# Performance work log

Hardware: AMD Instinct MI355X
Metric: run time of the kernel (lower is better)

Reference implementation:

```python
import jax, jax.numpy as jnp
import numpy as np

B = 128        # graph pairs per batch
NPG = 512      # nodes per graph (equal-size graphs -> dense batch is a reshape)
D = 64         # input feature dim
DEG = 16       # avg degree
FILTERS = [64, 32, 16]
RDIM = 10      # resize_dim
CCH = 8        # conv channels per similarity image
MLP = [32, 16, 8, 4, 1]


def _make_edges(rng, n_graphs, npg, deg):
    E = n_graphs * npg * deg
    off = np.repeat(np.arange(n_graphs, dtype=np.int64) * npg, npg * deg)
    src = rng.integers(0, npg, E) + off
    dst = rng.integers(0, npg, E) + off
    return jnp.asarray(np.stack([src, dst]), dtype=jnp.int32)


def setup_inputs() -> dict:
    key = jax.random.key(0)
    ks = jax.random.split(key, 40)
    rng = np.random.default_rng(0)
    N = B * NPG
    inp = {}
    inp['x_i'] = jax.random.normal(ks[0], (N, D), jnp.float32)
    inp['x_j'] = jax.random.normal(ks[1], (N, D), jnp.float32)
    # GCN weights
    dims = [D] + FILTERS
    k = 2
    for li in range(3):
        fi, fo = dims[li], dims[li + 1]
        inp[f'gcn_w{li}'] = jax.random.normal(ks[k], (fi, fo), jnp.float32) / np.sqrt(fi); k += 1
        inp[f'gcn_b{li}'] = jnp.zeros((fo,), jnp.float32)
    # Conv filters: one Conv2d(1->CCH, 3x3, SAME) per GNN layer, OIHW kernels
    for li in range(3):
        inp[f'conv_w{li}'] = jax.random.normal(ks[k], (CCH, 1, 3, 3), jnp.float32) / 3.0; k += 1
        inp[f'conv_b{li}'] = jnp.zeros((CCH,), jnp.float32)
    # MLP (Linear-ReLU stack) + scoring layer
    mdims = [3 * CCH * RDIM * RDIM] + MLP
    for li in range(len(MLP)):
        fi, fo = mdims[li], mdims[li + 1]
        inp[f'mlp_w{li}'] = jax.random.normal(ks[k], (fi, fo), jnp.float32) / np.sqrt(fi); k += 1
        inp[f'mlp_b{li}'] = jnp.zeros((fo,), jnp.float32)
    inp['score_w'] = jax.random.normal(ks[k], (1, 1), jnp.float32); k += 1
    inp['score_b'] = jnp.zeros((1,), jnp.float32)
    # Graph structure (int constants)
    inp['edge_index_i'] = _make_edges(rng, B, NPG, DEG)
    inp['edge_index_j'] = _make_edges(rng, B, NPG, DEG)
    batch = jnp.asarray(np.repeat(np.arange(B, dtype=np.int64), NPG), dtype=jnp.int32)
    inp['batch_i'] = batch
    inp['batch_j'] = batch
    return inp


def _gcn(x, ei, w, b):
    # PyG GCNConv: A_hat = D^-1/2 (A + I) D^-1/2 ; out = A_hat (x W) + b
    src, dst = ei[0], ei[1]
    n = x.shape[0]
    xw = x @ w
    deg = jax.ops.segment_sum(jnp.ones(ei.shape[1], xw.dtype), dst, num_segments=n) + 1.0
    inv = jax.lax.rsqrt(deg)
    msg = xw[src] * (inv[src] * inv[dst])[:, None]
    agg = jax.ops.segment_sum(msg, dst, num_segments=n)
    return agg + xw * (inv * inv)[:, None] + b


def _forward(x_i, x_j, gcn_w0, gcn_b0, gcn_w1, gcn_b1, gcn_w2, gcn_b2,
             conv_w0, conv_b0, conv_w1, conv_b1, conv_w2, conv_b2,
             mlp_w0, mlp_b0, mlp_w1, mlp_b1, mlp_w2, mlp_b2, mlp_w3, mlp_b3, mlp_w4, mlp_b4,
             score_w, score_b, edge_index_i, edge_index_j):
    gws = [(gcn_w0, gcn_b0), (gcn_w1, gcn_b1), (gcn_w2, gcn_b2)]
    cvs = [(conv_w0, conv_b0), (conv_w1, conv_b1), (conv_w2, conv_b2)]
    embs = []
    for li, (w, b) in enumerate(gws):
        x_i = _gcn(x_i, edge_index_i, w, b)
        x_j = _gcn(x_j, edge_index_j, w, b)
        if li != len(gws) - 1:  # activation + dropout (eval mode -> identity)
            x_i = jax.nn.relu(x_i)
            x_j = jax.nn.relu(x_j)
        h_i = x_i.reshape(B, NPG, -1)  # to_dense_batch (equal-size graphs)
        h_j = x_j.reshape(B, NPG, -1)
        sim = jnp.einsum('bnd,bmd->bnm', h_i, h_j)  # [B, NPG, NPG]
        simr = jax.image.resize(sim, (B, RDIM, RDIM), method='bilinear', antialias=False)
        cw, cb = cvs[li]
        y = jax.lax.conv_general_dilated(simr[:, None], cw, (1, 1), 'SAME')
        y = jax.nn.relu(y + cb[None, :, None, None])  # [B, CCH, RDIM, RDIM]
        embs.append(y.reshape(B, -1))
    feat = jnp.concatenate(embs, axis=1)  # [B, 3*CCH*RDIM*RDIM]
    for w, b in [(mlp_w0, mlp_b0), (mlp_w1, mlp_b1), (mlp_w2, mlp_b2), (mlp_w3, mlp_b3), (mlp_w4, mlp_b4)]:
        feat = jax.nn.relu(feat @ w + b)
    score = jax.nn.sigmoid(feat @ score_w + score_b)
    return score.reshape(-1)


def reference(x_i, x_j, gcn_w0, gcn_b0, gcn_w1, gcn_b1, gcn_w2, gcn_b2,
              conv_w0, conv_b0, conv_w1, conv_b1, conv_w2, conv_b2,
              mlp_w0, mlp_b0, mlp_w1, mlp_b1, mlp_w2, mlp_b2, mlp_w3, mlp_b3, mlp_w4, mlp_b4,
              score_w, score_b, edge_index_i, edge_index_j, batch_i, batch_j):
    # batch_i/batch_j are implicit in the block layout (equal-size graphs)
    return _forward(x_i, x_j, gcn_w0, gcn_b0, gcn_w1, gcn_b1, gcn_w2, gcn_b2,
                    conv_w0, conv_b0, conv_w1, conv_b1, conv_w2, conv_b2,
                    mlp_w0, mlp_b0, mlp_w1, mlp_b1, mlp_w2, mlp_b2, mlp_w3, mlp_b3, mlp_w4, mlp_b4,
                    score_w, score_b, edge_index_i, edge_index_j)
```

## Files before the change

kernel.cpp:

```cpp
#include <hip/hip_runtime.h>

typedef float fvec4 __attribute__((ext_vector_type(4)));

#define NN 65536
#define EE 1048576
#define BB 128
#define NPG 512
#define EPG 8192

template <int NQ, int FOUT, int COFF, bool RELU, bool LAST>
__device__ __forceinline__ void pass32(const fvec4* acc, fvec4* o,
                                       const float* __restrict__ bias,
                                       int node, int start, int count, float inv_v, int slot,
                                       fvec4* __restrict__ msgQ, const int* __restrict__ sids,
                                       float* __restrict__ hs, int hb) {
  {
    const int rb = node << 3;
    const int m = node & 7;
#pragma unroll
    for (int q = 0; q < NQ; ++q) msgQ[rb | ((q + m) & 7)] = acc[q] * inv_v;
  }
  __syncthreads();
  if (!LAST || slot >= 0) {
    fvec4 s[NQ];
#pragma unroll
    for (int q = 0; q < NQ; ++q) s[q] = fvec4{0.f, 0.f, 0.f, 0.f};
    int e = start;
    const int end = start + count;
    for (; e + 2 <= end; e += 2) {
      const int k0 = sids[e], k1 = sids[e + 1];
      const int b0 = k0 & ~7, b1 = k1 & ~7;
#pragma unroll
      for (int q = 0; q < NQ; ++q) s[q] += msgQ[b0 | ((q + k0) & 7)];
#pragma unroll
      for (int q = 0; q < NQ; ++q) s[q] += msgQ[b1 | ((q + k1) & 7)];
    }
    if (e < end) {
      const int k0 = sids[e];
      const int b0 = k0 & ~7;
#pragma unroll
      for (int q = 0; q < NQ; ++q) s[q] += msgQ[b0 | ((q + k0) & 7)];
    }
    const float i2 = inv_v * inv_v;
#pragma unroll
    for (int q = 0; q < NQ; ++q) {
#pragma unroll
      for (int j = 0; j < 4; ++j) {
        float ov = s[q][j] * inv_v + acc[q][j] * i2 + bias[COFF + q * 4 + j];
        if (RELU) ov = fmaxf(ov, 0.f);
        o[q][j] = ov;
      }
    }
    if (slot >= 0) {
      fvec4* hp = reinterpret_cast<fvec4*>(hs + ((size_t)hb + slot) * FOUT + COFF);
#pragma unroll
      for (int q = 0; q < NQ; ++q) hp[q] = o[q];
    }
  }
  __syncthreads();
}

__global__ __launch_bounds__(512)
void k_all(const float* __restrict__ x_i, const float* __restrict__ x_j,
           const float* __restrict__ gw0, const float* __restrict__ gb0,
           const float* __restrict__ gw1, const float* __restrict__ gb1,
           const float* __restrict__ gw2, const float* __restrict__ gb2,
           const int* __restrict__ ei, const int* __restrict__ ej,
           float* __restrict__ hs0, float* __restrict__ hs1, float* __restrict__ hs2) {
  __shared__ int sids[EPG];
  __shared__ fvec4 msgQ[NPG * 8];
  __shared__ int cnt[NPG];
  __shared__ int posb[NPG];
  __shared__ int nodeOf[NPG];
  __shared__ int bins[64];
  __shared__ int binpos[64];
  __shared__ int wsum[8];
  int* const dsts = reinterpret_cast<int*>(msgQ);

  const int side = blockIdx.x >> 7;
  const int g = blockIdx.x & 127;
  const float* __restrict__ x = side ? x_j : x_i;
  const int* __restrict__ eidx = side ? ej : ei;
  const int v = threadIdx.x;
  const int base = g * NPG;
  const int ebase = g * EPG;

  cnt[v] = 0;
  if (v < 64) bins[v] = 0;
  __syncthreads();
  for (int k = v; k < EPG; k += 512) {
    int d = eidx[EE + ebase + k] - base;
    dsts[k] = d;
    atomicAdd(&cnt[d], 1);
  }
  __syncthreads();

  const int count = cnt[v];
  const int deg = count > 63 ? 63 : count;
  atomicAdd(&bins[deg], 1);
  int xa = count;
  const int lane = v & 63;
#pragma unroll
  for (int d = 1; d < 64; d <<= 1) {
    int y = __shfl_up(xa, d, 64);
    if (lane >= d) xa += y;
  }
  const int wid = v >> 6;
  if (lane == 63) wsum[wid] = xa;
  __syncthreads();
  if (v < 64) {
    if (v == 0) {
      int a = 0;
#pragma unroll
      for (int i = 0; i < 8; ++i) { int tv = wsum[i]; wsum[i] = a; a += tv; }
    }
    int c = bins[v];
    int xb = c;
#pragma unroll
    for (int d = 1; d < 64; d <<= 1) {
      int y = __shfl_up(xb, d, 64);
      if (v >= d) xb += y;
    }
    binpos[v] = xb - c;
  }
  __syncthreads();
  const int start_v = xa - count + wsum[wid];
  posb[v] = start_v;
  {
    int rank = atomicAdd(&binpos[deg], 1);
    nodeOf[rank] = v;
  }
  __syncthreads();

  for (int k = v; k < EPG; k += 512) {
    int lv = eidx[ebase + k] - base;
    int p = atomicAdd(&posb[dsts[k]], 1);
    sids[p] = (lv << 3) | (lv & 7);
  }
  __syncthreads();

  const int node = nodeOf[v];
  const int ncount = cnt[node];
  const int nstart = posb[node] - ncount;
  const float inv_v = rsqrtf((float)ncount + 1.0f);

  constexpr int srows[20] = {25, 26, 76, 77, 127, 128, 178, 179, 229, 230,
                             281, 282, 332, 333, 383, 384, 434, 435, 485, 486};
  int slot = -1;
#pragma unroll
  for (int i = 0; i < 20; ++i)
    if (node == srows[i]) slot = i;
  const int hb = (side * BB + g) * 20;

  fvec4 a0[16];
#pragma unroll
  for (int q = 0; q < 16; ++q) a0[q] = fvec4{0.f, 0.f, 0.f, 0.f};
  {
    const fvec4* xv = reinterpret_cast<const fvec4*>(x + (size_t)(base + node) * 64);
#pragma unroll 1
    for (int k16 = 0; k16 < 4; ++k16) {
      fvec4 xq[4];
#pragma unroll
      for (int u = 0; u < 4; ++u) xq[u] = xv[4 * k16 + u];
#pragma unroll
      for (int u = 0; u < 4; ++u) {
#pragma unroll
        for (int j = 0; j < 4; ++j) {
          const float xk = xq[u][j];
          const fvec4* wr = reinterpret_cast<const fvec4*>(gw0 + (size_t)(16 * k16 + 4 * u + j) * 64);
#pragma unroll
          for (int q = 0; q < 16; ++q) a0[q] += xk * wr[q];
        }
      }
    }
  }

  fvec4 y1[8];
  {
    fvec4 o[8];
    pass32<8, 64, 0, true, false>(&a0[0], o, gb0, node, nstart, ncount, inv_v, slot, msgQ, sids, hs0, hb);
#pragma unroll
    for (int q = 0; q < 8; ++q) y1[q] = fvec4{0.f, 0.f, 0.f, 0.f};
#pragma unroll
    for (int f = 0; f < 32; ++f) {
      const float hf = o[f >> 2][f & 3];
      const fvec4* wr = reinterpret_cast<const fvec4*>(gw1 + (size_t)f * 32);
#pragma unroll
      for (int q = 0; q < 8; ++q) y1[q] += hf * wr[q];
    }
  }
  {
    fvec4 o[8];
    pass32<8, 64, 32, true, false>(&a0[8], o, gb0, node, nstart, ncount, inv_v, slot, msgQ, sids, hs0, hb);
#pragma unroll
    for (int f = 0; f < 32; ++f) {
      const float hf = o[f >> 2][f & 3];
      const fvec4* wr = reinterpret_cast<const fvec4*>(gw1 + (size_t)(32 + f) * 32);
#pragma unroll
      for (int q = 0; q < 8; ++q) y1[q] += hf * wr[q];
    }
  }

  fvec4 y2[4];
  {
    fvec4 o[8];
    pass32<8, 32, 0, true, false>(y1, o, gb1, node, nstart, ncount, inv_v, slot, msgQ, sids, hs1, hb);
#pragma unroll
    for (int q = 0; q < 4; ++q) y2[q] = fvec4{0.f, 0.f, 0.f, 0.f};
#pragma unroll
    for (int f = 0; f < 32; ++f) {
      const float hf = o[f >> 2][f & 3];
      const fvec4* wr = reinterpret_cast<const fvec4*>(gw2 + (size_t)f * 16);
#pragma unroll
      for (int q = 0; q < 4; ++q) y2[q] += hf * wr[q];
    }
  }

  {
    fvec4 o[4];
    pass32<4, 16, 0, false, true>(y2, o, gb2, node, nstart, ncount, inv_v, slot, msgQ, sids, hs2, hb);
  }
}

__global__ __launch_bounds__(256) void k_head(const float* __restrict__ hs0, const float* __restrict__ hs1,
                                              const float* __restrict__ hs2,
                                              const float* __restrict__ cw0, const float* __restrict__ cb0,
                                              const float* __restrict__ cw1, const float* __restrict__ cb1,
                                              const float* __restrict__ cw2, const float* __restrict__ cb2,
                                              const float* __restrict__ mw0, const float* __restrict__ mb0,
                                              const float* __restrict__ mw1, const float* __restrict__ mb1,
                                              const float* __restrict__ mw2, const float* __restrict__ mb2,
                                              const float* __restrict__ mw3, const float* __restrict__ mb3,
                                              const float* __restrict__ mw4, const float* __restrict__ mb4,
                                              const float* __restrict__ sw, const float* __restrict__ sb,
                                              float* __restrict__ out) {
  __shared__ float hi[2240];
  __shared__ float hj[2240];
  __shared__ float sim[400];
  __shared__ float simr[100];
  __shared__ float feat[2400];
  __shared__ float red[256];
  __shared__ float mbuf[60];
  const int b = blockIdx.x, t = threadIdx.x;

  for (int k = t; k < 1280; k += 256) {
    hi[k] = hs0[(size_t)(0 * BB + b) * 1280 + k];
    hj[k] = hs0[(size_t)(1 * BB + b) * 1280 + k];
  }
  for (int k = t; k < 640; k += 256) {
    hi[1280 + k] = hs1[(size_t)(0 * BB + b) * 640 + k];
    hj[1280 + k] = hs1[(size_t)(1 * BB + b) * 640 + k];
  }
  for (int k = t; k < 320; k += 256) {
    hi[1920 + k] = hs2[(size_t)(0 * BB + b) * 320 + k];
    hj[1920 + k] = hs2[(size_t)(1 * BB + b) * 320 + k];
  }
  __syncthreads();

  const int Fs[3] = {64, 32, 16};
  const int HOFF[3] = {0, 1280, 1920};
  const float* CW[3] = {cw0, cw1, cw2};
  const float* CB[3] = {cb0, cb1, cb2};

  for (int li = 0; li < 3; ++li) {
    const int F = Fs[li];
    const float* Hi = hi + HOFF[li];
    const float* Hj = hj + HOFF[li];
    for (int p = t; p < 400; p += 256) {
      int r = p / 20, cq = p % 20;
      float a = 0.0f;
      for (int d = 0; d < F; ++d) a += Hi[r * F + d] * Hj[cq * F + d];
      sim[p] = a;
    }
    __syncthreads();
    if (t < 100) {
      int oy = t / 10, ox = t % 10;
      float cy = (oy + 0.5f) * (512.0f / 10.0f) - 0.5f;
      float cx = (ox + 0.5f) * (512.0f / 10.0f) - 0.5f;
      float fy = cy - floorf(cy);
      float fx = cx - floorf(cx);
      int r0 = 2 * oy, c0 = 2 * ox;
      float s00 = sim[r0 * 20 + c0], s01 = sim[r0 * 20 + c0 + 1];
      float s10 = sim[(r0 + 1) * 20 + c0], s11 = sim[(r0 + 1) * 20 + c0 + 1];
      simr[t] = (1.0f - fy) * ((1.0f - fx) * s00 + fx * s01) + fy * ((1.0f - fx) * s10 + fx * s11);
    }
    __syncthreads();
    const float* cw = CW[li];
    const float* cb = CB[li];
    for (int idx = t; idx < 800; idx += 256) {
      int cch = idx / 100, rem = idx % 100, y = rem / 10, x = rem % 10;
      float a = cb[cch];
#pragma unroll
      for (int ky = 0; ky < 3; ++ky) {
#pragma unroll
        for (int kx = 0; kx < 3; ++kx) {
          int iy = y + ky - 1, ix = x + kx - 1;
          if (iy >= 0 && iy < 10 && ix >= 0 && ix < 10)
            a += cw[cch * 9 + ky * 3 + kx] * simr[iy * 10 + ix];
        }
      }
      feat[li * 800 + idx] = fmaxf(a, 0.0f);
    }
    __syncthreads();
  }

  {
    int f = t & 31, part = t >> 5;
    float a = 0.0f;
    int k0 = part * 300;
    for (int k = k0; k < k0 + 300; ++k) a += feat[k] * mw0[k * 32 + f];
    red[t] = a;
    __syncthreads();
    if (t < 32) {
      float s = mb0[t];
#pragma unroll
      for (int p = 0; p < 8; ++p) s += red[p * 32 + t];
      mbuf[t] = fmaxf(s, 0.0f);
    }
    __syncthreads();
  }
  if (t < 16) {
    float s = mb1[t];
    for (int k = 0; k < 32; ++k) s += mbuf[k] * mw1[k * 16 + t];
    mbuf[32 + t] = fmaxf(s, 0.0f);
  }
  __syncthreads();
  if (t < 8) {
    float s = mb2[t];
    for (int k = 0; k < 16; ++k) s += mbuf[32 + k] * mw2[k * 8 + t];
    mbuf[48 + t] = fmaxf(s, 0.0f);
  }
  __syncthreads();
  if (t < 4) {
    float s = mb3[t];
    for (int k = 0; k < 8; ++k) s += mbuf[48 + k] * mw3[k * 4 + t];
    mbuf[56 + t] = fmaxf(s, 0.0f);
  }
  __syncthreads();
  if (t == 0) {
    float s = mb4[0];
    for (int k = 0; k < 4; ++k) s += mbuf[56 + k] * mw4[k];
    s = fmaxf(s, 0.0f);
    float z = s * sw[0] + sb[0];
    out[b] = 1.0f / (1.0f + expf(-z));
  }
}

extern "C" void kernel_launch(void* const* d_in, const int* in_sizes, int n_in,
                              void* d_out, int out_size, void* d_ws, size_t ws_size,
                              hipStream_t stream) {
  (void)in_sizes; (void)n_in; (void)out_size; (void)ws_size;
  const float* x_i = (const float*)d_in[0];
  const float* x_j = (const float*)d_in[1];
  const float* gw0 = (const float*)d_in[2];
  const float* gb0 = (const float*)d_in[3];
  const float* gw1 = (const float*)d_in[4];
  const float* gb1 = (const float*)d_in[5];
  const float* gw2 = (const float*)d_in[6];
  const float* gb2 = (const float*)d_in[7];
  const float* cw0 = (const float*)d_in[8];
  const float* cb0 = (const float*)d_in[9];
  const float* cw1 = (const float*)d_in[10];
  const float* cb1 = (const float*)d_in[11];
  const float* cw2 = (const float*)d_in[12];
  const float* cb2 = (const float*)d_in[13];
  const float* mw0 = (const float*)d_in[14];
  const float* mb0 = (const float*)d_in[15];
  const float* mw1 = (const float*)d_in[16];
  const float* mb1 = (const float*)d_in[17];
  const float* mw2 = (const float*)d_in[18];
  const float* mb2 = (const float*)d_in[19];
  const float* mw3 = (const float*)d_in[20];
  const float* mb3 = (const float*)d_in[21];
  const float* mw4 = (const float*)d_in[22];
  const float* mb4 = (const float*)d_in[23];
  const float* scw = (const float*)d_in[24];
  const float* scb = (const float*)d_in[25];
  const int* ei = (const int*)d_in[26];
  const int* ej = (const int*)d_in[27];
  float* out = (float*)d_out;

  char* p = (char*)d_ws;
  auto take = [&](size_t bytes) {
    char* r = p;
    p += (bytes + 255) & ~(size_t)255;
    return r;
  };
  float* hs0 = (float*)take((size_t)2 * BB * 20 * 64 * 4);
  float* hs1 = (float*)take((size_t)2 * BB * 20 * 32 * 4);
  float* hs2 = (float*)take((size_t)2 * BB * 20 * 16 * 4);

  k_all<<<2 * BB, 512, 0, stream>>>(x_i, x_j, gw0, gb0, gw1, gb1, gw2, gb2,
                                    ei, ej, hs0, hs1, hs2);
  k_head<<<BB, 256, 0, stream>>>(hs0, hs1, hs2, cw0, cb0, cw1, cb1, cw2, cb2,
                                 mw0, mb0, mw1, mb1, mw2, mb2, mw3, mb3, mw4, mb4,
                                 scw, scb, out);
}
```

Baseline: 130.5 us.

## Store GCN neighbor messages in fp16 and merge layer-0 aggregation passes

Neighbor messages in shared memory are now packed as half2 instead of fp32, which halves LDS traffic per gather and lets both 32-feature halves of layer 0 be aggregated in one pass over the edge list using two buffers. The self-loop term is folded into the accumulator initialisation, and the sids encoding is changed to address the packed layout. This removes one edge traversal and a pair of barriers. The cost is fp16 rounding of the messages, which may affect accuracy.

Result: no change. 132.4 us (+1.5%).

```diff
diff --git a/kernel.cpp b/kernel.cpp
--- a/kernel.cpp
+++ b/kernel.cpp
@@ -1,6 +1,8 @@
 #include <hip/hip_runtime.h>
+#include <hip/hip_fp16.h>
 
 typedef float fvec4 __attribute__((ext_vector_type(4)));
+typedef int ivec4 __attribute__((ext_vector_type(4)));
 
 #define NN 65536
 #define EE 1048576
@@ -8,56 +10,32 @@
 #define NPG 512
 #define EPG 8192
 
-template <int NQ, int FOUT, int COFF, bool RELU, bool LAST>
-__device__ __forceinline__ void pass32(const fvec4* acc, fvec4* o,
-                                       const float* __restrict__ bias,
-                                       int node, int start, int count, float inv_v, int slot,
-                                       fvec4* __restrict__ msgQ, const int* __restrict__ sids,
-                                       float* __restrict__ hs, int hb) {
-  {
-    const int rb = node << 3;
-    const int m = node & 7;
-#pragma unroll
-    for (int q = 0; q < NQ; ++q) msgQ[rb | ((q + m) & 7)] = acc[q] * inv_v;
-  }
-  __syncthreads();
-  if (!LAST || slot >= 0) {
-    fvec4 s[NQ];
-#pragma unroll
-    for (int q = 0; q < NQ; ++q) s[q] = fvec4{0.f, 0.f, 0.f, 0.f};
-    int e = start;
-    const int end = start + count;
-    for (; e + 2 <= end; e += 2) {
-      const int k0 = sids[e], k1 = sids[e + 1];
-      const int b0 = k0 & ~7, b1 = k1 & ~7;
-#pragma unroll
-      for (int q = 0; q < NQ; ++q) s[q] += msgQ[b0 | ((q + k0) & 7)];
-#pragma unroll
-      for (int q = 0; q < NQ; ++q) s[q] += msgQ[b1 | ((q + k1) & 7)];
-    }
-    if (e < end) {
-      const int k0 = sids[e];
-      const int b0 = k0 & ~7;
-#pragma unroll
-      for (int q = 0; q < NQ; ++q) s[q] += msgQ[b0 | ((q + k0) & 7)];
-    }
-    const float i2 = inv_v * inv_v;
-#pragma unroll
-    for (int q = 0; q < NQ; ++q) {
-#pragma unroll
-      for (int j = 0; j < 4; ++j) {
-        float ov = s[q][j] * inv_v + acc[q][j] * i2 + bias[COFF + q * 4 + j];
-        if (RELU) ov = fmaxf(ov, 0.f);
-        o[q][j] = ov;
-      }
-    }
-    if (slot >= 0) {
-      fvec4* hp = reinterpret_cast<fvec4*>(hs + ((size_t)hb + slot) * FOUT + COFF);
-#pragma unroll
-      for (int q = 0; q < NQ; ++q) hp[q] = o[q];
-    }
-  }
-  __syncthreads();
+__device__ __forceinline__ int pk2(float a, float b) {
+  union { __half2 h; int i; } u; u.h = __floats2half2_rn(a, b); return u.i;
+}
+__device__ __forceinline__ float2 up2(int v) {
+  union { int i; __half2 h; } u; u.i = v; return __half22float2(u.h);
+}
+
+#define ACCQ(S, w) { float2 f_; \
+  f_ = up2((w)[0]); (S)[0][0] += f_.x; (S)[0][1] += f_.y; \
+  f_ = up2((w)[1]); (S)[0][2] += f_.x; (S)[0][3] += f_.y; \
+  f_ = up2((w)[2]); (S)[1][0] += f_.x; (S)[1][1] += f_.y; \
+  f_ = up2((w)[3]); (S)[1][2] += f_.x; (S)[1][3] += f_.y; }
+
+__device__ __forceinline__ void pub32(const fvec4* acc, float inv_v, int node, ivec4* buf) {
+  const int line = node >> 1;
+  const int m = ((node & 1) << 2) + (line & 7);
+  const int b = line << 3;
+#pragma unroll
+  for (int q = 0; q < 4; ++q) {
+    fvec4 a0 = acc[2 * q] * inv_v;
+    fvec4 a1 = acc[2 * q + 1] * inv_v;
+    ivec4 w;
+    w[0] = pk2(a0[0], a0[1]); w[1] = pk2(a0[2], a0[3]);
+    w[2] = pk2(a1[0], a1[1]); w[3] = pk2(a1[2], a1[3]);
+    buf[b | ((q + m) & 7)] = w;
+  }
 }
 
 __global__ __launch_bounds__(512)
@@ -68,14 +46,15 @@
            const int* __restrict__ ei, const int* __restrict__ ej,
            float* __restrict__ hs0, float* __restrict__ hs1, float* __restrict__ hs2) {
   __shared__ int sids[EPG];
-  __shared__ fvec4 msgQ[NPG * 8];
+  __shared__ ivec4 bufA[(NPG / 2) * 8];
+  __shared__ ivec4 bufB[(NPG / 2) * 8];
   __shared__ int cnt[NPG];
   __shared__ int posb[NPG];
   __shared__ int nodeOf[NPG];
   __shared__ int bins[64];
   __shared__ int binpos[64];
   __shared__ int wsum[8];
-  int* const dsts = reinterpret_cast<int*>(msgQ);
+  int* const dsts = reinterpret_cast<int*>(bufA);
 
   const int side = blockIdx.x >> 7;
   const int g = blockIdx.x & 127;
@@ -135,7 +114,9 @@
   for (int k = v; k < EPG; k += 512) {
     int lv = eidx[ebase + k] - base;
     int p = atomicAdd(&posb[dsts[k]], 1);
-    sids[p] = (lv << 3) | (lv & 7);
+    int line = lv >> 1;
+    int m = ((lv & 1) << 2) + (line & 7);
+    sids[p] = (line << 4) | m;
   }
   __syncthreads();
 
@@ -175,50 +156,123 @@
     }
   }
 
+  pub32(&a0[0], inv_v, node, bufA);
+  pub32(&a0[8], inv_v, node, bufB);
+  fvec4 sA[8], sB[8];
+#pragma unroll
+  for (int q = 0; q < 8; ++q) { sA[q] = a0[q] * inv_v; sB[q] = a0[8 + q] * inv_v; }
+  __syncthreads();
+
+  {
+    const int end = nstart + ncount;
+    for (int e = nstart; e < end; ++e) {
+      const int key = sids[e];
+      const int b = (key >> 1) & ~7;
+#pragma unroll
+      for (int q = 0; q < 4; ++q) {
+        const int idx = b | ((q + key) & 7);
+        const ivec4 wa = bufA[idx];
+        const ivec4 wb = bufB[idx];
+        ACCQ((&sA[2 * q]), wa)
+        ACCQ((&sB[2 * q]), wb)
+      }
+    }
+  }
+
   fvec4 y1[8];
-  {
-    fvec4 o[8];
-    pass32<8, 64, 0, true, false>(&a0[0], o, gb0, node, nstart, ncount, inv_v, slot, msgQ, sids, hs0, hb);
-#pragma unroll
-    for (int q = 0; q < 8; ++q) y1[q] = fvec4{0.f, 0.f, 0.f, 0.f};
-#pragma unroll
-    for (int f = 0; f < 32; ++f) {
-      const float hf = o[f >> 2][f & 3];
-      const fvec4* wr = reinterpret_cast<const fvec4*>(gw1 + (size_t)f * 32);
-#pragma unroll
-      for (int q = 0; q < 8; ++q) y1[q] += hf * wr[q];
-    }
-  }
-  {
-    fvec4 o[8];
-    pass32<8, 64, 32, true, false>(&a0[8], o, gb0, node, nstart, ncount, inv_v, slot, msgQ, sids, hs0, hb);
-#pragma unroll
-    for (int f = 0; f < 32; ++f) {
-      const float hf = o[f >> 2][f & 3];
-      const fvec4* wr = reinterpret_cast<const fvec4*>(gw1 + (size_t)(32 + f) * 32);
-#pragma unroll
-      for (int q = 0; q < 8; ++q) y1[q] += hf * wr[q];
-    }
-  }
-
+#pragma unroll
+  for (int p = 0; p < 8; ++p) y1[p] = fvec4{0.f, 0.f, 0.f, 0.f};
+  {
+    const fvec4* gb0v = reinterpret_cast<const fvec4*>(gb0);
+    fvec4* hp = reinterpret_cast<fvec4*>(hs0 + ((size_t)hb + slot) * 64);
+#pragma unroll
+    for (int q = 0; q < 16; ++q) {
+      fvec4 s = (q < 8) ? sA[q] : sB[q - 8];
+      fvec4 o = s * inv_v + gb0v[q];
+#pragma unroll
+      for (int j = 0; j < 4; ++j) o[j] = fmaxf(o[j], 0.f);
+      if (slot >= 0) hp[q] = o;
+#pragma unroll
+      for (int j = 0; j < 4; ++j) {
+        const float hf = o[j];
+        const fvec4* wr = reinterpret_cast<const fvec4*>(gw1 + (size_t)(q * 4 + j) * 32);
+#pragma unroll
+        for (int p = 0; p < 8; ++p) y1[p] += hf * wr[p];
+      }
+    }
+  }
+  __syncthreads();
+
+  pub32(y1, inv_v, node, bufA);
+  fvec4 s1[8];
+#pragma unroll
+  for (int q = 0; q < 8; ++q) s1[q] = y1[q] * inv_v;
+  __syncthreads();
+  {
+    const int end = nstart + ncount;
+    for (int e = nstart; e < end; ++e) {
+      const int key = sids[e];
+      const int b = (key >> 1) & ~7;
+#pragma unroll
+      for (int q = 0; q < 4; ++q) {
+        const ivec4 w = bufA[b | ((q + key) & 7)];
+        ACCQ((&s1[2 * q]), w)
+      }
+    }
+  }
   fvec4 y2[4];
-  {
-    fvec4 o[8];
-    pass32<8, 32, 0, true, false>(y1, o, gb1, node, nstart, ncount, inv_v, slot, msgQ, sids, hs1, hb);
-#pragma unroll
-    for (int q = 0; q < 4; ++q) y2[q] = fvec4{0.f, 0.f, 0.f, 0.f};
-#pragma unroll
-    for (int f = 0; f < 32; ++f) {
-      const float hf = o[f >> 2][f & 3];
-      const fvec4* wr = reinterpret_cast<const fvec4*>(gw2 + (size_t)f * 16);
-#pragma unroll
-      for (int q = 0; q < 4; ++q) y2[q] += hf * wr[q];
-    }
-  }
-
-  {
-    fvec4 o[4];
-    pass32<4, 16, 0, false, true>(y2, o, gb2, node, nstart, ncount, inv_v, slot, msgQ, sids, hs2, hb);
+#pragma unroll
+  for (int p = 0; p < 4; ++p) y2[p] = fvec4{0.f, 0.f, 0.f, 0.f};
+  {
+    const fvec4* gb1v = reinterpret_cast<const fvec4*>(gb1);
+    fvec4* hp = reinterpret_cast<fvec4*>(hs1 + ((size_t)hb + slot) * 32);
+#pragma unroll
+    for (int q = 0; q < 8; ++q) {
+      fvec4 o = s1[q] * inv_v + gb1v[q];
+#pragma unroll
+      for (int j = 0; j < 4; ++j) o[j] = fmaxf(o[j], 0.f);
+      if (slot >= 0) hp[q] = o;
+#pragma unroll
+      for (int j = 0; j < 4; ++j) {
+        const float hf = o[j];
+        const fvec4* wr = reinterpret_cast<const fvec4*>(gw2 + (size_t)(q * 4 + j) * 16);
+#pragma unroll
+        for (int p = 0; p < 4; ++p) y2[p] += hf * wr[p];
+      }
+    }
+  }
+
+  {
+    const int line = node >> 1;
+    const int m = ((node & 1) << 2) + (line & 7);
+    const int b = line << 3;
+    fvec4 q0 = y2[0] * inv_v, q1 = y2[1] * inv_v, q2 = y2[2] * inv_v, q3 = y2[3] * inv_v;
+    ivec4 w0, w1;
+    w0[0] = pk2(q0[0], q0[1]); w0[1] = pk2(q0[2], q0[3]);
+    w0[2] = pk2(q1[0], q1[1]); w0[3] = pk2(q1[2], q1[3]);
+    w1[0] = pk2(q2[0], q2[1]); w1[1] = pk2(q2[2], q2[3]);
+    w1[2] = pk2(q3[0], q3[1]); w1[3] = pk2(q3[2], q3[3]);
+    bufB[b | (m & 7)] = w0;
+    bufB[b | ((1 + m) & 7)] = w1;
+  }
+  fvec4 s2[4];
+#pragma unroll
+  for (int q = 0; q < 4; ++q) s2[q] = y2[q] * inv_v;
+  __syncthreads();
+  if (slot >= 0) {
+    const int end = nstart + ncount;
+    for (int e = nstart; e < end; ++e) {
+      const int key = sids[e];
+      const int b = (key >> 1) & ~7;
+      const ivec4 w0 = bufB[b | (key & 7)];
+      const ivec4 w1 = bufB[b | ((1 + key) & 7)];
+      ACCQ((&s2[0]), w0)
+      ACCQ((&s2[2]), w1)
+    }
+    const fvec4* gb2v = reinterpret_cast<const fvec4*>(gb2);
+    fvec4* hp = reinterpret_cast<fvec4*>(hs2 + ((size_t)hb + slot) * 16);
+#pragma unroll
+    for (int q = 0; q < 4; ++q) hp[q] = s2[q] * inv_v + gb2v[q];
   }
 }
 
```
